# Optimization experiments

Hardware: AMD Instinct MI355X
Metric: run time of the kernel (lower is better)

## Reference

```python
import jax, jax.numpy as jnp
import numpy as np

B, L, D = 4, 8192, 512


def _normalize(v):
    # F.normalize: v / max(||v||, 1e-12)
    n = jnp.linalg.norm(v, axis=-1, keepdims=True)
    return v / jnp.maximum(n, 1e-12)


def setup_inputs() -> dict:
    key = jax.random.key(0)
    k1, k2, k3, k4 = jax.random.split(key, 4)
    return {
        "hidden_states": jax.random.normal(k1, (B, L, D), jnp.float32),
        "residual": jax.random.normal(k2, (B, L, D), jnp.float32),
        "q_weight": jax.random.normal(k3, (D, D), jnp.float32) * 0.02,
        "k_weight": jax.random.normal(k4, (D, D), jnp.float32) * 0.02,
        "det_state": jnp.zeros((B, D), jnp.float32),
    }


def reference(hidden_states, residual, q_weight, k_weight, det_state):
    Bs, Ls, Ds = hidden_states.shape
    # ---- CosineSimRouter.prob_boundary ----
    q = _normalize(hidden_states[:, :-1] @ q_weight.T)   # (B, L-1, D)
    k = _normalize(hidden_states[:, 1:] @ k_weight.T)    # (B, L-1, D)
    cos_sim = jnp.einsum('bld,bld->bl', q, k)            # (B, L-1)
    prob = jnp.concatenate(
        [jnp.ones((Bs, 1), jnp.float32), jnp.clip((1.0 - cos_sim) / 2.0, 0.0, 1.0)],
        axis=1)                                           # (B, L); prob[:,0]=1 (state=None path)
    token_mask = prob > 0.5                               # (B, L)

    # ---- Tokenizer: compact boundary positions (pad M -> L, static shape) ----
    counts = token_mask.sum(axis=1)                       # (B,)
    order = jnp.argsort(~token_mask, axis=1)              # stable: True-mask indices first, in order
    valid = jnp.arange(Ls)[None, :] < counts[:, None]     # (B, L)
    chunked = jnp.take_along_axis(hidden_states, order[..., None], axis=1)
    chunked = chunked * valid[..., None]                  # (B, L, D)
    chunk_probs = jnp.take_along_axis(prob, order, axis=1) * valid  # (B, L)

    # ---- DeTokenizer: EMA associative scan over compacted chunks ----
    decay = jnp.clip(1.0 - chunk_probs, 0.0, 1.0)
    # pad positions have chunk_probs=0 -> decay=1 -> state carried unchanged
    a = jnp.broadcast_to(decay[..., None], (Bs, Ls, Ds))
    b = (1.0 - decay)[..., None] * chunked
    b = b.at[:, 0].add(a[:, 0] * det_state)

    def comb(x, y):  # x earlier, y later: (a2*a1, a2*b1 + b2)
        ax, bx = x
        ay, by = y
        return ax * ay, ay * bx + by

    _, ema_out = jax.lax.associative_scan(comb, (a, b), axis=1)
    ema_out = ema_out * valid[..., None]                  # zero padded chunk slots

    # broadcast back to full sequence via cumulative chunk indexing
    chunk_idx = jnp.cumsum(token_mask.astype(jnp.int32), axis=1) - 1  # (B, L)
    ci = jnp.clip(chunk_idx, 0, Ls - 1)
    long_states = jnp.take_along_axis(ema_out, ci[..., None], axis=1)
    long_states = long_states * (chunk_idx >= 0)[..., None]

    # STE coefficient: forward == 1 (grad flows through max(1-p, p) in bwd)
    coef_raw = jnp.maximum(1.0 - prob, prob)
    coef = coef_raw + jax.lax.stop_gradient(1.0 - coef_raw)
    long_states = long_states * coef[..., None]

    output = residual + long_states                       # (B, L, D)
    return output
```

## Files before the change

kernel.cpp:

```cpp
#include <hip/hip_runtime.h>
#include <hip/hip_bf16.h>
#include <math.h>

#define B_  4
#define L_  8192
#define D_  512

#define BM   128
#define NCT  4
#define NRT  (L_ / BM)
#define KW   64
#define NSTAGE (D_ / KW)

#define CHUNK 64
#define NCHUNK (L_ / CHUNK)

#define MAXFIX 16380
#define FIX_TAU 1.0e-3f
#define FROWS 8

typedef short bf16x8 __attribute__((ext_vector_type(8)));
typedef float f32x4 __attribute__((ext_vector_type(4)));
typedef unsigned short u16;
typedef unsigned int u32;

__device__ __forceinline__ u32 pk2(float lo, float hi) {
    __hip_bfloat162 v = __float22bfloat162_rn(float2{lo, hi});
    union { __hip_bfloat162 b; u32 u; } cv; cv.b = v;
    return cv.u;
}

__global__ __launch_bounds__(256) void prep_w(
    const float* __restrict__ wq, const float* __restrict__ wk,
    u16* __restrict__ qh, u16* __restrict__ kh,
    float* __restrict__ wqt, float* __restrict__ wkt,
    int* __restrict__ fix_cnt)
{
    __shared__ float tile[64][65];
    const int bi = blockIdx.x;
    const int bj = blockIdx.y;
    const int t = threadIdx.x;
    if (bi == 0 && bj == 0 && t == 0) *fix_cnt = 0;
    const int c0 = bi * 64, k0 = bj * 64;
    const float* src = wq; float* dst = wqt; u16* dsth = qh;
#pragma unroll
    for (int m = 0; m < 2; ++m) {
        __syncthreads();
#pragma unroll
        for (int it = 0; it < 4; ++it) {
            int r = it * 16 + (t >> 4);
            int cc = (t & 15) * 4;
            float4 v = *(const float4*)(src + (size_t)(c0 + r) * D_ + k0 + cc);
            tile[r][cc] = v.x; tile[r][cc + 1] = v.y;
            tile[r][cc + 2] = v.z; tile[r][cc + 3] = v.w;
            uint2 hv; hv.x = pk2(v.x, v.y); hv.y = pk2(v.z, v.w);
            *(uint2*)(dsth + (size_t)(c0 + r) * D_ + k0 + cc) = hv;
        }
        __syncthreads();
#pragma unroll
        for (int it = 0; it < 4; ++it) {
            int cl = t & 63;
            int kq = it * 4 + (t >> 6);
            float4 v;
            v.x = tile[cl][kq * 4 + 0]; v.y = tile[cl][kq * 4 + 1];
            v.z = tile[cl][kq * 4 + 2]; v.w = tile[cl][kq * 4 + 3];
            size_t o = ((size_t)((k0 >> 2) + kq) * 512 + (c0 + cl)) * 4;
            *(float4*)(dst + o) = v;
        }
        src = wk; dst = wkt; dsth = kh;
    }
}

__global__ __launch_bounds__(256, 2) void qk_mfma(
    const float* __restrict__ h,
    const u16* __restrict__ wqh, const u16* __restrict__ wkh,
    float* __restrict__ part)
{
    const int bid = blockIdx.x;
    const int swz = (bid & 7) * 128 + (bid >> 3);
    const int ct = swz & 3, rt = (swz >> 2) & 63, b = swz >> 8;
    const int t = threadIdx.x, wid = t >> 6, lane = t & 63;
    const int l15 = lane & 15, l4 = lane >> 4;

    __shared__ __align__(16) u16 ah[129 * 64];
    __shared__ float red[4][BM][3];

    const int r0 = rt * BM;
    const float* hb = h + (size_t)b * L_ * D_;

    const int tr = t >> 4, q = t & 15;
    const float* gp = hb + (size_t)(r0 + tr) * D_ + q * 4;
    const int re = (r0 + BM > L_ - 1) ? (L_ - 1) : (r0 + BM);
    const float* gpe = hb + (size_t)re * D_ + q * 4;
    const int dbase = tr * 64 + (((q >> 1) ^ (tr & 7)) * 8) + ((q & 1) * 4);
    const int dE = 128 * 64 + ((t >> 1) * 8) + ((t & 1) * 4);

    const int colb = ct * 128 + wid * 32;
    const u16* bq0 = wqh + (size_t)(colb + l15) * D_ + l4 * 8;
    const u16* bq1 = bq0 + (size_t)16 * D_;
    const u16* bk0 = wkh + (size_t)(colb + l15) * D_ + l4 * 8;
    const u16* bk1 = bk0 + (size_t)16 * D_;

    int aoff[8];
#pragma unroll
    for (int rf = 0; rf < 8; ++rf) {
        int R = rf * 16 + l15;
        aoff[rf] = R * 64 + ((l4 ^ (R & 7)) * 8);
    }
    const int aoffE = 128 * 64 + l4 * 8;

    f32x4 accq[8][2], acck[8][2], ackl[2];
    const f32x4 zero = {0.f, 0.f, 0.f, 0.f};
#pragma unroll
    for (int rf = 0; rf < 8; ++rf) {
        accq[rf][0] = zero; accq[rf][1] = zero;
        acck[rf][0] = zero; acck[rf][1] = zero;
    }
    ackl[0] = zero; ackl[1] = zero;

    float4 A0, A1, A2, A3, A4, A5, A6, A7;
    float4 AE = {0.f, 0.f, 0.f, 0.f};

#define LOADA(S) do { const int _o = (S) * KW;                      \
    A0 = *(const float4*)(gp + _o);                                 \
    A1 = *(const float4*)(gp + _o + 8192);                          \
    A2 = *(const float4*)(gp + _o + 16384);                         \
    A3 = *(const float4*)(gp + _o + 24576);                         \
    A4 = *(const float4*)(gp + _o + 32768);                         \
    A5 = *(const float4*)(gp + _o + 40960);                         \
    A6 = *(const float4*)(gp + _o + 49152);                         \
    A7 = *(const float4*)(gp + _o + 57344);                         \
    if (t < 16) AE = *(const float4*)(gpe + _o); } while (0)

#define ST1(J, AV) { uint2 _h; _h.x = pk2(AV.x, AV.y); _h.y = pk2(AV.z, AV.w); \
    *(uint2*)(&ah[dbase + (J) * 1024]) = _h; }

    LOADA(0);
    for (int s = 0; s < NSTAGE; ++s) {
        __builtin_amdgcn_sched_barrier(0);
        __builtin_amdgcn_s_barrier();
        __builtin_amdgcn_sched_barrier(0);

        ST1(0, A0) ST1(1, A1) ST1(2, A2) ST1(3, A3)
        ST1(4, A4) ST1(5, A5) ST1(6, A6) ST1(7, A7)
        if (t < 16) { uint2 _h; _h.x = pk2(AE.x, AE.y); _h.y = pk2(AE.z, AE.w);
                      *(uint2*)(&ah[dE]) = _h; }

        const int so = s * KW;
        bf16x8 q00 = *(const bf16x8*)(bq0 + so);
        bf16x8 q01 = *(const bf16x8*)(bq0 + so + 32);
        bf16x8 q10 = *(const bf16x8*)(bq1 + so);
        bf16x8 q11 = *(const bf16x8*)(bq1 + so + 32);
        bf16x8 k00 = *(const bf16x8*)(bk0 + so);
        bf16x8 k01 = *(const bf16x8*)(bk0 + so + 32);
        bf16x8 k10 = *(const bf16x8*)(bk1 + so);
        bf16x8 k11 = *(const bf16x8*)(bk1 + so + 32);

        if (s + 1 < NSTAGE) LOADA(s + 1);

        asm volatile("s_waitcnt lgkmcnt(0)" ::: "memory");
        __builtin_amdgcn_sched_barrier(0);
        __builtin_amdgcn_s_barrier();
        __builtin_amdgcn_sched_barrier(0);

#pragma unroll
        for (int kk = 0; kk < 2; ++kk) {
            bf16x8 fq0 = kk ? q01 : q00;
            bf16x8 fq1 = kk ? q11 : q10;
            bf16x8 fk0 = kk ? k01 : k00;
            bf16x8 fk1 = kk ? k11 : k10;
#pragma unroll
            for (int rf = 0; rf < 8; ++rf) {
                bf16x8 a = *(const bf16x8*)(&ah[aoff[rf] ^ (kk * 32)]);
                accq[rf][0] = __builtin_amdgcn_mfma_f32_16x16x32_bf16(a, fq0, accq[rf][0], 0, 0, 0);
                accq[rf][1] = __builtin_amdgcn_mfma_f32_16x16x32_bf16(a, fq1, accq[rf][1], 0, 0, 0);
                acck[rf][0] = __builtin_amdgcn_mfma_f32_16x16x32_bf16(a, fk0, acck[rf][0], 0, 0, 0);
                acck[rf][1] = __builtin_amdgcn_mfma_f32_16x16x32_bf16(a, fk1, acck[rf][1], 0, 0, 0);
            }
            bf16x8 al = *(const bf16x8*)(&ah[aoffE ^ (kk * 32)]);
            ackl[0] = __builtin_amdgcn_mfma_f32_16x16x32_bf16(al, fk0, ackl[0], 0, 0, 0);
            ackl[1] = __builtin_amdgcn_mfma_f32_16x16x32_bf16(al, fk1, ackl[1], 0, 0, 0);
        }
    }
#undef LOADA
#undef ST1

#pragma unroll
    for (int rf = 0; rf < 8; ++rf) {
#pragma unroll
        for (int reg = 0; reg < 4; ++reg) {
            float pq = 0.f, pk = 0.f, pd = 0.f;
#pragma unroll
            for (int cf = 0; cf < 2; ++cf) {
                float qv = accq[rf][cf][reg];
                float kv = acck[rf][cf][reg];
                pq += qv * qv;
                pk += kv * kv;
                float ksh;
                if (reg < 3) {
                    ksh = acck[rf][cf][reg + 1];
                } else {
                    float up = __shfl(acck[rf][cf][0], (lane + 16) & 63);
                    float nx0 = (rf < 7) ? acck[rf + 1][cf][0] : ackl[cf][0];
                    float nx = __shfl(nx0, l15);
                    ksh = (l4 == 3) ? nx : up;
                }
                pd += qv * ksh;
            }
#pragma unroll
            for (int off = 1; off < 16; off <<= 1) {
                pq += __shfl_xor(pq, off);
                pk += __shfl_xor(pk, off);
                pd += __shfl_xor(pd, off);
            }
            if (l15 == 0) {
                int row = rf * 16 + l4 * 4 + reg;
                red[wid][row][0] = pq;
                red[wid][row][1] = pk;
                red[wid][row][2] = pd;
            }
        }
    }
    __syncthreads();
    if (t < BM) {
        float pq = red[0][t][0] + red[1][t][0] + red[2][t][0] + red[3][t][0];
        float pk = red[0][t][1] + red[1][t][1] + red[2][t][1] + red[3][t][1];
        float pd = red[0][t][2] + red[1][t][2] + red[2][t][2] + red[3][t][2];
        size_t o = (((size_t)ct * B_ + b) * L_ + (r0 + t)) * 3;
        part[o + 0] = pq; part[o + 1] = pk; part[o + 2] = pd;
    }
}

__global__ __launch_bounds__(256) void cos_reduce(
    const float* __restrict__ part, float* __restrict__ p,
    int* __restrict__ fix_cnt, int* __restrict__ fix_list)
{
    int idx = blockIdx.x * 256 + threadIdx.x;
    if (idx >= B_ * L_) return;
    int b = idx / L_;
    int tp = idx % L_;
    if (tp == 0) { p[idx] = 1.0f; return; }
    int l = tp - 1;
    float nq = 0.f, nk = 0.f, dt = 0.f;
#pragma unroll
    for (int ct = 0; ct < NCT; ++ct) {
        size_t o = (((size_t)ct * B_ + b) * L_ + l) * 3;
        nq += part[o + 0];
        dt += part[o + 2];
        nk += part[o + 4];
    }
    float qn = sqrtf(nq); if (qn < 1e-12f) qn = 1e-12f;
    float kn = sqrtf(nk); if (kn < 1e-12f) kn = 1e-12f;
    float cs = dt / (qn * kn);
    float pr = 0.5f * (1.0f - cs);
    pr = fminf(fmaxf(pr, 0.0f), 1.0f);
    p[idx] = pr;
    if (fabsf(cs) < FIX_TAU) {
        int slot = atomicAdd(fix_cnt, 1);
        if (slot < MAXFIX) fix_list[slot] = idx;
    }
}

__global__ __launch_bounds__(256) void fixup_main(
    const float* __restrict__ h,
    const float* __restrict__ wqt, const float* __restrict__ wkt,
    const int* __restrict__ fix_cnt, const int* __restrict__ fix_list,
    float* __restrict__ part_fix)
{
    __shared__ float hq[FROWS][D_];
    __shared__ float hk[FROWS][D_];
    __shared__ float red[FROWS][3][4];
    const int t = threadIdx.x, wid = t >> 6, lane = t & 63;
    const int kh = lane >> 5;
    int n = *fix_cnt; if (n > MAXFIX) n = MAXFIX;
    const int ntiles = (n + FROWS - 1) / FROWS;
    const int nitems = ntiles * 4;

    for (int item = blockIdx.x; item < nitems; item += gridDim.x) {
        const int tile = item >> 2;
        const int cs = item & 3;
        __syncthreads();
#pragma unroll
        for (int r = 0; r < FROWS; ++r) {
            int s = tile * FROWS + r;
            int idx = fix_list[s < n ? s : 0];
            int bb = idx >> 13;
            int tp = idx & (L_ - 1);
            const float* hr = h + ((size_t)bb * L_ + (tp - 1)) * D_;
            ((float2*)hq[r])[t] = ((const float2*)hr)[t];
            ((float2*)hk[r])[t] = ((const float2*)(hr + D_))[t];
        }
        __syncthreads();

        const int c = cs * 128 + wid * 32 + (lane & 31);
        float qa0, qa1, qa2, qa3, qa4, qa5, qa6, qa7;
        float ka0, ka1, ka2, ka3, ka4, ka5, ka6, ka7;
        qa0=qa1=qa2=qa3=qa4=qa5=qa6=qa7=0.f;
        ka0=ka1=ka2=ka3=ka4=ka5=ka6=ka7=0.f;

        const int k0 = kh * 64;
        float4 wv = *(const float4*)(wqt + ((size_t)k0 * 512 + c) * 4);
        float4 xv = *(const float4*)(wkt + ((size_t)k0 * 512 + c) * 4);
#pragma unroll 4
        for (int kq = k0; kq < k0 + 64; ++kq) {
            const int kn = (kq + 1 < k0 + 64) ? kq + 1 : kq;
            float4 wn = *(const float4*)(wqt + ((size_t)kn * 512 + c) * 4);
            float4 xn = *(const float4*)(wkt + ((size_t)kn * 512 + c) * 4);
#define FROW(R, QA, KA) { \
            float4 hv = *(const float4*)(&hq[R][kq * 4]); \
            float4 kv = *(const float4*)(&hk[R][kq * 4]); \
            QA += hv.x*wv.x + hv.y*wv.y + hv.z*wv.z + hv.w*wv.w; \
            KA += kv.x*xv.x + kv.y*xv.y + kv.z*xv.z + kv.w*xv.w; }
            FROW(0, qa0, ka0) FROW(1, qa1, ka1) FROW(2, qa2, ka2) FROW(3, qa3, ka3)
            FROW(4, qa4, ka4) FROW(5, qa5, ka5) FROW(6, qa6, ka6) FROW(7, qa7, ka7)
#undef FROW
            wv = wn; xv = xn;
        }

#define REDROW(R, QA, KA) { \
        float qf = QA + __shfl_xor(QA, 32); \
        float kf = KA + __shfl_xor(KA, 32); \
        float pq = qf * qf, pk = kf * kf, pd = qf * kf; \
        for (int off = 1; off < 32; off <<= 1) { \
            pq += __shfl_xor(pq, off); \
            pk += __shfl_xor(pk, off); \
            pd += __shfl_xor(pd, off); \
        } \
        if (lane == 0) { red[R][0][wid] = pq; red[R][1][wid] = pk; red[R][2][wid] = pd; } }
        REDROW(0, qa0, ka0) REDROW(1, qa1, ka1) REDROW(2, qa2, ka2) REDROW(3, qa3, ka3)
        REDROW(4, qa4, ka4) REDROW(5, qa5, ka5) REDROW(6, qa6, ka6) REDROW(7, qa7, ka7)
#undef REDROW
        __syncthreads();
        if (t < FROWS) {
            int s = tile * FROWS + t;
            if (s < n) {
                float* pp = part_fix + ((size_t)s * 4 + cs) * 3;
                pp[0] = red[t][0][0] + red[t][0][1] + red[t][0][2] + red[t][0][3];
                pp[1] = red[t][1][0] + red[t][1][1] + red[t][1][2] + red[t][1][3];
                pp[2] = red[t][2][0] + red[t][2][1] + red[t][2][2] + red[t][2][3];
            }
        }
    }
}

__global__ __launch_bounds__(256) void fixup_final(
    const int* __restrict__ fix_cnt, const int* __restrict__ fix_list,
    const float* __restrict__ part_fix, float* __restrict__ p)
{
    int n = *fix_cnt; if (n > MAXFIX) n = MAXFIX;
    for (int s = blockIdx.x * 256 + threadIdx.x; s < n; s += gridDim.x * 256) {
        float nq = 0.f, nk = 0.f, dt = 0.f;
#pragma unroll
        for (int cs = 0; cs < 4; ++cs) {
            const float* pp = part_fix + ((size_t)s * 4 + cs) * 3;
            nq += pp[0]; nk += pp[1]; dt += pp[2];
        }
        float qn = sqrtf(nq); if (qn < 1e-12f) qn = 1e-12f;
        float kn = sqrtf(nk); if (kn < 1e-12f) kn = 1e-12f;
        float cs2 = dt / (qn * kn);
        float pr = 0.5f * (1.0f - cs2);
        pr = fminf(fmaxf(pr, 0.0f), 1.0f);
        p[fix_list[s]] = pr;
    }
}

__global__ __launch_bounds__(256) void scan_a(
    const float* __restrict__ h, const float* __restrict__ p,
    float* __restrict__ Bc, float* __restrict__ Ac)
{
    const int t = threadIdx.x;
    const int c = blockIdx.x, b = blockIdx.y;
    const int l0 = c * CHUNK;
    const float* pb = p + (size_t)b * L_ + l0;
    const float2* hb = (const float2*)(h + ((size_t)b * L_ + l0) * D_) + t;

    float2 st = {0.f, 0.f};
    float ap = 1.f;
#pragma unroll 4
    for (int i = 0; i < CHUNK; ++i) {
        float pr = pb[i];
        float2 hv = hb[(size_t)i * 256];
        bool sel = pr > 0.5f;
        float a = sel ? 1.f - pr : 1.f;
        float g = sel ? pr : 0.f;
        st.x = a * st.x + g * hv.x;
        st.y = a * st.y + g * hv.y;
        ap *= a;
    }
    ((float2*)Bc)[((size_t)b * NCHUNK + c) * 256 + t] = st;
    if (t == 0) Ac[b * NCHUNK + c] = ap;
}

__global__ __launch_bounds__(256) void scan_b(
    const float* __restrict__ Ac, const float* __restrict__ Bc,
    const float* __restrict__ det, float* __restrict__ carry)
{
    const int t = threadIdx.x;
    const int b = blockIdx.x;
    const float* acb = Ac + b * NCHUNK;
    const float2* bcb = (const float2*)Bc + (size_t)b * NCHUNK * 256 + t;
    float2* cb = (float2*)carry + (size_t)b * NCHUNK * 256 + t;
    float2 st = ((const float2*)det)[(size_t)b * 256 + t];

    float a0 = acb[0], a1 = acb[1], a2 = acb[2], a3 = acb[3];
    float2 b0 = bcb[0], b1 = bcb[256], b2 = bcb[512], b3 = bcb[768];
    for (int g = 0; g < NCHUNK / 4; ++g) {
        const int nc = (g + 1 < NCHUNK / 4) ? (g + 1) * 4 : g * 4;
        float an0 = acb[nc], an1 = acb[nc + 1], an2 = acb[nc + 2], an3 = acb[nc + 3];
        float2 bn0 = bcb[(size_t)nc * 256],        bn1 = bcb[(size_t)(nc + 1) * 256];
        float2 bn2 = bcb[(size_t)(nc + 2) * 256],  bn3 = bcb[(size_t)(nc + 3) * 256];
        const size_t c0 = (size_t)g * 4 * 256;
        cb[c0]       = st; st.x = a0 * st.x + b0.x; st.y = a0 * st.y + b0.y;
        cb[c0 + 256] = st; st.x = a1 * st.x + b1.x; st.y = a1 * st.y + b1.y;
        cb[c0 + 512] = st; st.x = a2 * st.x + b2.x; st.y = a2 * st.y + b2.y;
        cb[c0 + 768] = st; st.x = a3 * st.x + b3.x; st.y = a3 * st.y + b3.y;
        a0 = an0; a1 = an1; a2 = an2; a3 = an3;
        b0 = bn0; b1 = bn1; b2 = bn2; b3 = bn3;
    }
}

__global__ __launch_bounds__(256) void scan_c(
    const float* __restrict__ h, const float* __restrict__ p,
    const float* __restrict__ res, const float* __restrict__ carry,
    float* __restrict__ out)
{
    const int t = threadIdx.x;
    const int c = blockIdx.x, b = blockIdx.y;
    const int l0 = c * CHUNK;
    const float* pb = p + (size_t)b * L_ + l0;
    const size_t base = ((size_t)b * L_ + l0) * 256 + t;
    const float2* hb = (const float2*)h + base;
    const float2* rb = (const float2*)res + base;
    float2* ob = (float2*)out + base;

    float2 st = ((const float2*)carry)[((size_t)b * NCHUNK + c) * 256 + t];
#pragma unroll 4
    for (int i = 0; i < CHUNK; ++i) {
        float pr = pb[i];
        float2 hv = hb[(size_t)i * 256];
        float2 rv = rb[(size_t)i * 256];
        bool sel = pr > 0.5f;
        float a = sel ? 1.f - pr : 1.f;
        float g = sel ? pr : 0.f;
        st.x = a * st.x + g * hv.x;
        st.y = a * st.y + g * hv.y;
        float2 ov; ov.x = rv.x + st.x; ov.y = rv.y + st.y;
        ob[(size_t)i * 256] = ov;
    }
}

extern "C" void kernel_launch(void* const* d_in, const int* in_sizes, int n_in,
                              void* d_out, int out_size, void* d_ws, size_t ws_size,
                              hipStream_t stream)
{
    const float* h   = (const float*)d_in[0];
    const float* res = (const float*)d_in[1];
    const float* wq  = (const float*)d_in[2];
    const float* wk  = (const float*)d_in[3];
    const float* det = (const float*)d_in[4];
    float* out = (float*)d_out;

    float* ws = (float*)d_ws;
    float* part  = ws;
    float* p     = part + (size_t)NCT * B_ * L_ * 3;
    float* Ac    = p + (size_t)B_ * L_;
    float* Bc    = Ac + (size_t)B_ * NCHUNK;
    float* carry = Bc + (size_t)B_ * NCHUNK * D_;
    int*  fix_cnt  = (int*)(carry + (size_t)B_ * NCHUNK * D_);
    int*  fix_list = fix_cnt + 4;
    u16* wqh = (u16*)(fix_list + MAXFIX);
    u16* wkh = wqh + (size_t)D_ * D_;
    float* wqt = (float*)(wkh + (size_t)D_ * D_);
    float* wkt = wqt + (size_t)D_ * D_;
    float* part_fix = wkt + (size_t)D_ * D_;

    prep_w<<<dim3(8, 8), 256, 0, stream>>>(wq, wk, wqh, wkh, wqt, wkt, fix_cnt);
    qk_mfma<<<NCT * NRT * B_, 256, 0, stream>>>(h, wqh, wkh, part);
    cos_reduce<<<(B_ * L_ + 255) / 256, 256, 0, stream>>>(part, p, fix_cnt, fix_list);
    fixup_main<<<512, 256, 0, stream>>>(h, wqt, wkt, fix_cnt, fix_list, part_fix);
    fixup_final<<<64, 256, 0, stream>>>(fix_cnt, fix_list, part_fix, p);
    scan_a<<<dim3(NCHUNK, B_), 256, 0, stream>>>(h, p, Bc, Ac);
    scan_b<<<B_, 256, 0, stream>>>(Ac, Bc, det, carry);
    scan_c<<<dim3(NCHUNK, B_), 256, 0, stream>>>(h, p, res, carry, out);
}
```

Measured before the change: 180.8 us.

## Pre-convert activations to bf16 and stream GEMM tiles via async global-to-LDS loads

Adds a pass that converts hidden_states to bf16 into the output buffer, which is used as scratch. The projection GEMM then double-buffers A tiles in LDS using global_load_lds, so the next stage loads while the current one computes, with no register staging or conversion inside the loop. The fixup kernel also moves to 8 column slices with a 4-way k split and twice as many blocks. The cost is an extra full read and half-size write of the activations, plus a dependence on the output buffer being free until the scan writes it.

Measured after the change: 173.1 us. -4.2%, faster.

```diff
diff --git a/kernel.cpp b/kernel.cpp
--- a/kernel.cpp
+++ b/kernel.cpp
@@ -18,6 +18,7 @@
 #define MAXFIX 16380
 #define FIX_TAU 1.0e-3f
 #define FROWS 8
+#define NSLICE 8
 
 typedef short bf16x8 __attribute__((ext_vector_type(8)));
 typedef float f32x4 __attribute__((ext_vector_type(4)));
@@ -28,6 +29,22 @@
     __hip_bfloat162 v = __float22bfloat162_rn(float2{lo, hi});
     union { __hip_bfloat162 b; u32 u; } cv; cv.b = v;
     return cv.u;
+}
+
+#define GLOAD_LDS(g, l) __builtin_amdgcn_global_load_lds( \
+    (__attribute__((address_space(1))) void*)(g),         \
+    (__attribute__((address_space(3))) void*)(l), 16, 0, 0)
+
+__global__ __launch_bounds__(256) void conv_h(
+    const float* __restrict__ h, u16* __restrict__ h16)
+{
+    size_t i = ((size_t)blockIdx.x * 256 + threadIdx.x) * 8;
+    float4 a = *(const float4*)(h + i);
+    float4 b = *(const float4*)(h + i + 4);
+    uint4 v;
+    v.x = pk2(a.x, a.y); v.y = pk2(a.z, a.w);
+    v.z = pk2(b.x, b.y); v.w = pk2(b.z, b.w);
+    *(uint4*)(h16 + i) = v;
 }
 
 __global__ __launch_bounds__(256) void prep_w(
@@ -72,7 +89,7 @@
 }
 
 __global__ __launch_bounds__(256, 2) void qk_mfma(
-    const float* __restrict__ h,
+    const u16* __restrict__ h16,
     const u16* __restrict__ wqh, const u16* __restrict__ wkh,
     float* __restrict__ part)
 {
@@ -82,18 +99,19 @@
     const int t = threadIdx.x, wid = t >> 6, lane = t & 63;
     const int l15 = lane & 15, l4 = lane >> 4;
 
-    __shared__ __align__(16) u16 ah[129 * 64];
+    __shared__ __align__(16) u16 ah[2][129 * 64];
     __shared__ float red[4][BM][3];
 
     const int r0 = rt * BM;
-    const float* hb = h + (size_t)b * L_ * D_;
-
-    const int tr = t >> 4, q = t & 15;
-    const float* gp = hb + (size_t)(r0 + tr) * D_ + q * 4;
+    const u16* hb = h16 + (size_t)b * L_ * D_;
+
+    const int rl0 = wid * 32 + (lane >> 3);
+    const int csw = ((lane & 7) ^ (rl0 & 7)) * 8;
+    const u16* gA = hb + (size_t)(r0 + rl0) * D_ + csw;
+    const int dstw = wid * 32 * 64;
+
     const int re = (r0 + BM > L_ - 1) ? (L_ - 1) : (r0 + BM);
-    const float* gpe = hb + (size_t)re * D_ + q * 4;
-    const int dbase = tr * 64 + (((q >> 1) ^ (tr & 7)) * 8) + ((q & 1) * 4);
-    const int dE = 128 * 64 + ((t >> 1) * 8) + ((t & 1) * 4);
+    const u16* gpe = hb + (size_t)re * D_;
 
     const int colb = ct * 128 + wid * 32;
     const u16* bq0 = wqh + (size_t)(colb + l15) * D_ + l4 * 8;
@@ -118,33 +136,24 @@
     }
     ackl[0] = zero; ackl[1] = zero;
 
-    float4 A0, A1, A2, A3, A4, A5, A6, A7;
-    float4 AE = {0.f, 0.f, 0.f, 0.f};
-
-#define LOADA(S) do { const int _o = (S) * KW;                      \
-    A0 = *(const float4*)(gp + _o);                                 \
-    A1 = *(const float4*)(gp + _o + 8192);                          \
-    A2 = *(const float4*)(gp + _o + 16384);                         \
-    A3 = *(const float4*)(gp + _o + 24576);                         \
-    A4 = *(const float4*)(gp + _o + 32768);                         \
-    A5 = *(const float4*)(gp + _o + 40960);                         \
-    A6 = *(const float4*)(gp + _o + 49152);                         \
-    A7 = *(const float4*)(gp + _o + 57344);                         \
-    if (t < 16) AE = *(const float4*)(gpe + _o); } while (0)
-
-#define ST1(J, AV) { uint2 _h; _h.x = pk2(AV.x, AV.y); _h.y = pk2(AV.z, AV.w); \
-    *(uint2*)(&ah[dbase + (J) * 1024]) = _h; }
-
-    LOADA(0);
+#define STAGE_ISSUE(S, BUF) do { const int _o = (S) * KW;      \
+    GLOAD_LDS(gA + _o,         &ah[BUF][dstw]);                \
+    GLOAD_LDS(gA + _o + 4096,  &ah[BUF][dstw + 512]);          \
+    GLOAD_LDS(gA + _o + 8192,  &ah[BUF][dstw + 1024]);         \
+    GLOAD_LDS(gA + _o + 12288, &ah[BUF][dstw + 1536]); } while (0)
+
+    STAGE_ISSUE(0, 0);
+    uint2 er = {0, 0};
+    if (t < 16) er = *(const uint2*)(gpe + t * 4);
+    if (t < 16) *(uint2*)(&ah[0][128 * 64 + t * 4]) = er;
+    __syncthreads();
+
+    int cur = 0;
     for (int s = 0; s < NSTAGE; ++s) {
-        __builtin_amdgcn_sched_barrier(0);
-        __builtin_amdgcn_s_barrier();
-        __builtin_amdgcn_sched_barrier(0);
-
-        ST1(0, A0) ST1(1, A1) ST1(2, A2) ST1(3, A3)
-        ST1(4, A4) ST1(5, A5) ST1(6, A6) ST1(7, A7)
-        if (t < 16) { uint2 _h; _h.x = pk2(AE.x, AE.y); _h.y = pk2(AE.z, AE.w);
-                      *(uint2*)(&ah[dE]) = _h; }
+        if (s + 1 < NSTAGE) {
+            STAGE_ISSUE(s + 1, cur ^ 1);
+            if (t < 16) er = *(const uint2*)(gpe + (s + 1) * KW + t * 4);
+        }
 
         const int so = s * KW;
         bf16x8 q00 = *(const bf16x8*)(bq0 + so);
@@ -156,13 +165,7 @@
         bf16x8 k10 = *(const bf16x8*)(bk1 + so);
         bf16x8 k11 = *(const bf16x8*)(bk1 + so + 32);
 
-        if (s + 1 < NSTAGE) LOADA(s + 1);
-
-        asm volatile("s_waitcnt lgkmcnt(0)" ::: "memory");
-        __builtin_amdgcn_sched_barrier(0);
-        __builtin_amdgcn_s_barrier();
-        __builtin_amdgcn_sched_barrier(0);
-
+        const u16* ab = ah[cur];
 #pragma unroll
         for (int kk = 0; kk < 2; ++kk) {
             bf16x8 fq0 = kk ? q01 : q00;
@@ -171,19 +174,23 @@
             bf16x8 fk1 = kk ? k11 : k10;
 #pragma unroll
             for (int rf = 0; rf < 8; ++rf) {
-                bf16x8 a = *(const bf16x8*)(&ah[aoff[rf] ^ (kk * 32)]);
+                bf16x8 a = *(const bf16x8*)(ab + (aoff[rf] ^ (kk * 32)));
                 accq[rf][0] = __builtin_amdgcn_mfma_f32_16x16x32_bf16(a, fq0, accq[rf][0], 0, 0, 0);
                 accq[rf][1] = __builtin_amdgcn_mfma_f32_16x16x32_bf16(a, fq1, accq[rf][1], 0, 0, 0);
                 acck[rf][0] = __builtin_amdgcn_mfma_f32_16x16x32_bf16(a, fk0, acck[rf][0], 0, 0, 0);
                 acck[rf][1] = __builtin_amdgcn_mfma_f32_16x16x32_bf16(a, fk1, acck[rf][1], 0, 0, 0);
             }
-            bf16x8 al = *(const bf16x8*)(&ah[aoffE ^ (kk * 32)]);
+            bf16x8 al = *(const bf16x8*)(ab + (aoffE ^ (kk * 32)));
             ackl[0] = __builtin_amdgcn_mfma_f32_16x16x32_bf16(al, fk0, ackl[0], 0, 0, 0);
             ackl[1] = __builtin_amdgcn_mfma_f32_16x16x32_bf16(al, fk1, ackl[1], 0, 0, 0);
         }
-    }
-#undef LOADA
-#undef ST1
+
+        if (s + 1 < NSTAGE && t < 16)
+            *(uint2*)(&ah[cur ^ 1][128 * 64 + t * 4]) = er;
+        __syncthreads();
+        cur ^= 1;
+    }
+#undef STAGE_ISSUE
 
 #pragma unroll
     for (int rf = 0; rf < 8; ++rf) {
@@ -271,14 +278,14 @@
     __shared__ float hk[FROWS][D_];
     __shared__ float red[FROWS][3][4];
     const int t = threadIdx.x, wid = t >> 6, lane = t & 63;
-    const int kh = lane >> 5;
+    const int col16 = lane & 15, kpart = lane >> 4;
     int n = *fix_cnt; if (n > MAXFIX) n = MAXFIX;
     const int ntiles = (n + FROWS - 1) / FROWS;
-    const int nitems = ntiles * 4;
+    const int nitems = ntiles * NSLICE;
 
     for (int item = blockIdx.x; item < nitems; item += gridDim.x) {
-        const int tile = item >> 2;
-        const int cs = item & 3;
+        const int tile = item >> 3;
+        const int cs = item & 7;
         __syncthreads();
 #pragma unroll
         for (int r = 0; r < FROWS; ++r) {
@@ -292,18 +299,18 @@
         }
         __syncthreads();
 
-        const int c = cs * 128 + wid * 32 + (lane & 31);
+        const int c = cs * 64 + wid * 16 + col16;
         float qa0, qa1, qa2, qa3, qa4, qa5, qa6, qa7;
         float ka0, ka1, ka2, ka3, ka4, ka5, ka6, ka7;
         qa0=qa1=qa2=qa3=qa4=qa5=qa6=qa7=0.f;
         ka0=ka1=ka2=ka3=ka4=ka5=ka6=ka7=0.f;
 
-        const int k0 = kh * 64;
+        const int k0 = kpart * 32;
         float4 wv = *(const float4*)(wqt + ((size_t)k0 * 512 + c) * 4);
         float4 xv = *(const float4*)(wkt + ((size_t)k0 * 512 + c) * 4);
 #pragma unroll 4
-        for (int kq = k0; kq < k0 + 64; ++kq) {
-            const int kn = (kq + 1 < k0 + 64) ? kq + 1 : kq;
+        for (int kq = k0; kq < k0 + 32; ++kq) {
+            const int kn = (kq + 1 < k0 + 32) ? kq + 1 : kq;
             float4 wn = *(const float4*)(wqt + ((size_t)kn * 512 + c) * 4);
             float4 xn = *(const float4*)(wkt + ((size_t)kn * 512 + c) * 4);
 #define FROW(R, QA, KA) { \
@@ -318,14 +325,13 @@
         }
 
 #define REDROW(R, QA, KA) { \
-        float qf = QA + __shfl_xor(QA, 32); \
-        float kf = KA + __shfl_xor(KA, 32); \
+        float qf = QA; qf += __shfl_xor(qf, 16); qf += __shfl_xor(qf, 32); \
+        float kf = KA; kf += __shfl_xor(kf, 16); kf += __shfl_xor(kf, 32); \
         float pq = qf * qf, pk = kf * kf, pd = qf * kf; \
-        for (int off = 1; off < 32; off <<= 1) { \
-            pq += __shfl_xor(pq, off); \
-            pk += __shfl_xor(pk, off); \
-            pd += __shfl_xor(pd, off); \
-        } \
+        pq += __shfl_xor(pq, 1); pk += __shfl_xor(pk, 1); pd += __shfl_xor(pd, 1); \
+        pq += __shfl_xor(pq, 2); pk += __shfl_xor(pk, 2); pd += __shfl_xor(pd, 2); \
+        pq += __shfl_xor(pq, 4); pk += __shfl_xor(pk, 4); pd += __shfl_xor(pd, 4); \
+        pq += __shfl_xor(pq, 8); pk += __shfl_xor(pk, 8); pd += __shfl_xor(pd, 8); \
         if (lane == 0) { red[R][0][wid] = pq; red[R][1][wid] = pk; red[R][2][wid] = pd; } }
         REDROW(0, qa0, ka0) REDROW(1, qa1, ka1) REDROW(2, qa2, ka2) REDROW(3, qa3, ka3)
         REDROW(4, qa4, ka4) REDROW(5, qa5, ka5) REDROW(6, qa6, ka6) REDROW(7, qa7, ka7)
@@ -334,7 +340,7 @@
         if (t < FROWS) {
             int s = tile * FROWS + t;
             if (s < n) {
-                float* pp = part_fix + ((size_t)s * 4 + cs) * 3;
+                float* pp = part_fix + ((size_t)s * NSLICE + cs) * 3;
                 pp[0] = red[t][0][0] + red[t][0][1] + red[t][0][2] + red[t][0][3];
                 pp[1] = red[t][1][0] + red[t][1][1] + red[t][1][2] + red[t][1][3];
                 pp[2] = red[t][2][0] + red[t][2][1] + red[t][2][2] + red[t][2][3];
@@ -351,8 +357,8 @@
     for (int s = blockIdx.x * 256 + threadIdx.x; s < n; s += gridDim.x * 256) {
         float nq = 0.f, nk = 0.f, dt = 0.f;
 #pragma unroll
-        for (int cs = 0; cs < 4; ++cs) {
-            const float* pp = part_fix + ((size_t)s * 4 + cs) * 3;
+        for (int cs = 0; cs < NSLICE; ++cs) {
+            const float* pp = part_fix + ((size_t)s * NSLICE + cs) * 3;
             nq += pp[0]; nk += pp[1]; dt += pp[2];
         }
         float qn = sqrtf(nq); if (qn < 1e-12f) qn = 1e-12f;
@@ -460,6 +466,8 @@
     const float* det = (const float*)d_in[4];
     float* out = (float*)d_out;
 
+    u16* h16 = (u16*)d_out;
+
     float* ws = (float*)d_ws;
     float* part  = ws;
     float* p     = part + (size_t)NCT * B_ * L_ * 3;
@@ -474,10 +482,11 @@
     float* wkt = wqt + (size_t)D_ * D_;
     float* part_fix = wkt + (size_t)D_ * D_;
 
+    conv_h<<<(B_ * L_ * D_) / (256 * 8), 256, 0, stream>>>(h, h16);
     prep_w<<<dim3(8, 8), 256, 0, stream>>>(wq, wk, wqh, wkh, wqt, wkt, fix_cnt);
-    qk_mfma<<<NCT * NRT * B_, 256, 0, stream>>>(h, wqh, wkh, part);
+    qk_mfma<<<NCT * NRT * B_, 256, 0, stream>>>(h16, wqh, wkh, part);
     cos_reduce<<<(B_ * L_ + 255) / 256, 256, 0, stream>>>(part, p, fix_cnt, fix_list);
-    fixup_main<<<512, 256, 0, stream>>>(h, wqt, wkt, fix_cnt, fix_list, part_fix);
+    fixup_main<<<1024, 256, 0, stream>>>(h, wqt, wkt, fix_cnt, fix_list, part_fix);
     fixup_final<<<64, 256, 0, stream>>>(fix_cnt, fix_list, part_fix, p);
     scan_a<<<dim3(NCHUNK, B_), 256, 0, stream>>>(h, p, Bc, Ac);
     scan_b<<<B_, 256, 0, stream>>>(Ac, Bc, det, carry);
```
